# Kernel tuning notes

Hardware: AMD Instinct MI355X
Metric: run time of the kernel (lower is better)

Reference implementation:

```python
import jax, jax.numpy as jnp
import numpy as np

EMB_DIM = 1024
H = 16
HEAD_DIM = EMB_DIM // H
B = 2
S = 2048  # enc and dec seq len
LN_EPS = 1e-5


def setup_inputs() -> dict:
    key = jax.random.key(0)
    ks = jax.random.split(key, 8)
    scale_in = 1.0 / np.sqrt(EMB_DIM)
    scale_o = 1.0 / np.sqrt(H * HEAD_DIM)
    return {
        "enc_out": jax.random.normal(ks[0], (B, S, EMB_DIM), jnp.float32),
        "dec_out": jax.random.normal(ks[1], (B, S, EMB_DIM), jnp.float32),
        # stacked per-head projections, equivalent to h separate Linear(emb_dim, head_dim, bias=False)
        "Wq": jax.random.uniform(ks[2], (H, EMB_DIM, HEAD_DIM), jnp.float32, -scale_in, scale_in),
        "Wk": jax.random.uniform(ks[3], (H, EMB_DIM, HEAD_DIM), jnp.float32, -scale_in, scale_in),
        "Wv": jax.random.uniform(ks[4], (H, EMB_DIM, HEAD_DIM), jnp.float32, -scale_in, scale_in),
        "Wo": jax.random.uniform(ks[5], (H * HEAD_DIM, EMB_DIM), jnp.float32, -scale_o, scale_o),
        "gamma": jnp.ones((EMB_DIM,), jnp.float32),
        "beta": jnp.zeros((EMB_DIM,), jnp.float32),
    }


def reference(enc_out, dec_out, Wq, Wk, Wv, Wo, gamma, beta):
    d = Wq.shape[-1]
    # per-head projections, batched over heads (same math as the Python loop)
    q = jnp.einsum('bse,hed->bhsd', dec_out, Wq)   # queries from decoder
    k = jnp.einsum('bte,hed->bhtd', enc_out, Wk)   # keys from encoder
    v = jnp.einsum('bte,hed->bhtd', enc_out, Wv)   # values from encoder
    scores = jnp.einsum('bhsd,bhtd->bhst', q, k) / jnp.sqrt(jnp.asarray(d, q.dtype))
    att = jax.nn.softmax(scores, axis=-1)
    ctx = jnp.einsum('bhst,bhtd->bhsd', att, v)
    b, h, s, hd = ctx.shape
    ctx = ctx.transpose(0, 2, 1, 3).reshape(b, s, h * hd)  # concat heads along feature dim
    transformed = ctx @ Wo  # dropout is identity in eval mode
    x = dec_out + transformed
    mu = jnp.mean(x, axis=-1, keepdims=True)
    var = jnp.mean(jnp.square(x - mu), axis=-1, keepdims=True)
    return (x - mu) * jax.lax.rsqrt(var + LN_EPS) * gamma + beta
```

## Files before the change

### kernel.cpp

```cpp
#include <hip/hip_runtime.h>
#include <hip/hip_bf16.h>

#define EMB   1024
#define NH    16
#define HD    64
#define SEQ   2048
#define SA    72

typedef __attribute__((ext_vector_type(8))) short          bf16x8;
typedef __attribute__((ext_vector_type(8))) unsigned short us8;
typedef __attribute__((ext_vector_type(4))) float          f32x4;

__device__ __forceinline__ float u2f(unsigned short u) {
    return __uint_as_float(((unsigned)u) << 16);
}
__device__ __forceinline__ unsigned short f2u(float f) {
    __hip_bfloat16 b = __float2bfloat16(f);
    return *reinterpret_cast<unsigned short*>(&b);
}
__device__ __forceinline__ bool detect_bf16(const void* gamma) {
    return ((const unsigned short*)gamma)[0] == 0x3F80;
}
__device__ __forceinline__ f32x4 fzero() {
    f32x4 v; v.x = v.y = v.z = v.w = 0.f; return v;
}
__device__ __forceinline__ void ld16f(const void* p, size_t idx, bool isbf, float* o) {
    if (isbf) {
        const unsigned short* b = (const unsigned short*)p + idx;
        us8 v0 = *(const us8*)b, v1 = *(const us8*)(b + 8);
        #pragma unroll
        for (int i = 0; i < 8; ++i) { o[i] = u2f(v0[i]); o[8 + i] = u2f(v1[i]); }
    } else {
        const float* f = (const float*)p + idx;
        #pragma unroll
        for (int i = 0; i < 4; ++i) {
            float4 v = *(const float4*)(f + 4 * i);
            o[4*i] = v.x; o[4*i+1] = v.y; o[4*i+2] = v.z; o[4*i+3] = v.w;
        }
    }
}
__device__ __forceinline__ float ld1f(const void* p, size_t i, bool isbf) {
    return isbf ? u2f(((const unsigned short*)p)[i]) : ((const float*)p)[i];
}
__device__ __forceinline__ float4 ld4(const void* p, size_t idx, bool isbf) {
    if (isbf) {
        ushort4 t = *reinterpret_cast<const ushort4*>((const unsigned short*)p + idx);
        return make_float4(u2f(t.x), u2f(t.y), u2f(t.z), u2f(t.w));
    }
    return *reinterpret_cast<const float4*>((const float*)p + idx);
}
__device__ __forceinline__ us8 pk8(const float* s) {
    us8 v;
    #pragma unroll
    for (int i = 0; i < 8; ++i) v[i] = f2u(s[i]);
    return v;
}
__device__ __forceinline__ f32x4 mfma16(bf16x8 a, bf16x8 b, f32x4 c) {
    return __builtin_amdgcn_mfma_f32_16x16x32_bf16(a, b, c, 0, 0, 0);
}
__device__ __forceinline__ bf16x8 mk8(unsigned w0, unsigned w1, unsigned w2, unsigned w3) {
    union { unsigned u[4]; bf16x8 v; } x;
    x.u[0] = w0; x.u[1] = w1; x.u[2] = w2; x.u[3] = w3;
    return x.v;
}
__device__ __forceinline__ float fexp2(float x) {
    return __builtin_amdgcn_exp2f(x);
}
__device__ __forceinline__ unsigned cvtpk(float lo, float hi) {
    unsigned r;
    asm("v_cvt_pk_bf16_f32 %0, %1, %2" : "=v"(r) : "v"(lo), "v"(hi));
    return r;
}
__device__ __forceinline__ void gl_lds16(const unsigned short* g, unsigned short* l) {
    __builtin_amdgcn_global_load_lds(
        (const __attribute__((address_space(1))) void*)g,
        (__attribute__((address_space(3))) void*)l,
        16, 0, 0);
}

#define QSCALE 0.18033688f

__global__ __launch_bounds__(256) void convert_x_kernel(
    const void* __restrict__ dec, const void* __restrict__ enc,
    const void* __restrict__ gamma, unsigned short* __restrict__ xb)
{
    const bool isbf = detect_bf16(gamma);
    const size_t HALF = (size_t)4096 * 1024;
    size_t idx = ((size_t)blockIdx.x * 256 + threadIdx.x) * 16;
    const void* src; size_t off;
    if (idx < HALF) { src = dec; off = idx; } else { src = enc; off = idx - HALF; }
    float buf[16];
    ld16f(src, off, isbf, buf);
    *(us8*)&xb[idx]     = pk8(buf);
    *(us8*)&xb[idx + 8] = pk8(buf + 8);
}

__global__ __launch_bounds__(256) void transpose_w_kernel(
    const void* __restrict__ Wq, const void* __restrict__ Wk,
    const void* __restrict__ Wv, const void* __restrict__ gamma,
    unsigned short* __restrict__ wt)
{
    const bool isbf = detect_bf16(gamma);
    const int which = blockIdx.z, h = blockIdx.y, e0 = blockIdx.x * 64;
    const void* W = (which == 0) ? Wq : (which == 1 ? Wk : Wv);

    __shared__ unsigned short T[64][SA];
    const int sr = threadIdx.x >> 2, sc = (threadIdx.x & 3) * 16;

    float buf[16];
    ld16f(W, ((size_t)h * EMB + e0 + sr) * HD + sc, isbf, buf);
    #pragma unroll
    for (int i = 0; i < 16; ++i) T[sc + i][sr] = f2u(buf[i]);
    __syncthreads();
    us8 v0 = *(const us8*)&T[sr][sc];
    us8 v1 = *(const us8*)&T[sr][sc + 8];
    size_t o = (((size_t)which * NH + h) * HD + sr) * EMB + e0 + sc;
    *(us8*)&wt[o] = v0;
    *(us8*)&wt[o + 8] = v1;
}

__global__ __launch_bounds__(256) void transpose_wo_kernel(
    const void* __restrict__ Wo, const void* __restrict__ gamma,
    unsigned short* __restrict__ wot)
{
    const bool isbf = detect_bf16(gamma);
    const int n0 = blockIdx.x * 64, k0 = blockIdx.y * 64;
    __shared__ unsigned short T[64][SA];
    const int sr = threadIdx.x >> 2, sc = (threadIdx.x & 3) * 16;

    float buf[16];
    ld16f(Wo, (size_t)(k0 + sr) * EMB + n0 + sc, isbf, buf);
    #pragma unroll
    for (int i = 0; i < 16; ++i) T[sc + i][sr] = f2u(buf[i]);
    __syncthreads();
    us8 v0 = *(const us8*)&T[sr][sc];
    us8 v1 = *(const us8*)&T[sr][sc + 8];
    size_t o = (size_t)(n0 + sr) * EMB + k0 + sc;
    *(us8*)&wot[o] = v0;
    *(us8*)&wot[o + 8] = v1;
}

__global__ __launch_bounds__(256) void qkv_kernel(
    const unsigned short* __restrict__ xb,
    const unsigned short* __restrict__ wt,
    unsigned short* __restrict__ qo, unsigned short* __restrict__ ko,
    unsigned short* __restrict__ vt)
{
    const int id = blockIdx.x;
    const int xcd = id & 7, sl = id >> 3;
    const int m_t = xcd * 4 + (sl & 3);
    const int n_t = sl >> 2;
    const int m0 = m_t * 128, n0g = n_t * 128;
    const int which = n0g >> 10;
    const int nloc = n0g & 1023;
    const unsigned short* X = xb + ((which == 0) ? (size_t)0 : (size_t)4096 * 1024);

    __shared__ unsigned short smem[17408];
    unsigned short* const ldsA = smem;
    unsigned short* const ldsB = smem + 8192;

    const int tid = threadIdx.x, wv = tid >> 6, lane = tid & 63;
    const int lq = lane >> 4, lm = lane & 15;
    const int mw = (wv & 1) * 64, nw = (wv >> 1) * 64;

    const unsigned short* Wb = wt + (size_t)(which * 1024 + nloc) * EMB;

    const int seg0 = wv * 4;
    const int srow = lane >> 3;
    const int su   = (lane & 7) ^ srow;
    const unsigned short* aP[4];
    const unsigned short* bP[4];
    #pragma unroll
    for (int q = 0; q < 4; ++q) {
        const int s = seg0 + q;
        aP[q] = X  + (size_t)(m0 + 8 * s + srow) * EMB + su * 8;
        bP[q] = Wb + (size_t)(8 * s + srow) * EMB + su * 8;
    }

    f32x4 acc[4][4];
    #pragma unroll
    for (int i = 0; i < 4; ++i)
        #pragma unroll
        for (int j = 0; j < 4; ++j) acc[i][j] = fzero();

    const int xa = lm & 7;

    for (int k0 = 0; k0 < EMB; k0 += 64) {
        #pragma unroll
        for (int q = 0; q < 4; ++q) {
            gl_lds16(aP[q] + k0, ldsA + (seg0 + q) * 512);
            gl_lds16(bP[q] + k0, ldsB + (seg0 + q) * 512);
        }
        asm volatile("s_waitcnt vmcnt(0)" ::: "memory");
        __syncthreads();

        #pragma unroll
        for (int st = 0; st < 2; ++st) {
            const int u = (st * 4 + lq) ^ xa;
            bf16x8 af[4], bq[4];
            #pragma unroll
            for (int i = 0; i < 4; ++i)
                af[i] = *(const bf16x8*)(ldsA + (mw + i * 16 + lm) * 64 + u * 8);
            #pragma unroll
            for (int j = 0; j < 4; ++j)
                bq[j] = *(const bf16x8*)(ldsB + (nw + j * 16 + lm) * 64 + u * 8);
            #pragma unroll
            for (int i = 0; i < 4; ++i)
                #pragma unroll
                for (int j = 0; j < 4; ++j)
                    acc[i][j] = mfma16(af[i], bq[j], acc[i][j]);
        }
        __syncthreads();
    }

    const int b = m0 >> 11, s0 = m0 & (SEQ - 1);
    const float osc = (which == 0) ? QSCALE : 1.0f;
    if (which != 2) {
        unsigned short* Y = which ? ko : qo;
        #pragma unroll
        for (int i = 0; i < 4; ++i)
            #pragma unroll
            for (int j = 0; j < 4; ++j)
                #pragma unroll
                for (int r = 0; r < 4; ++r) {
                    int m = mw + i * 16 + lq * 4 + r;
                    int n = nloc + nw + j * 16 + lm;
                    int h = n >> 6, d = n & 63;
                    Y[(((size_t)b * NH + h) * SEQ + s0 + m) * HD + d] = f2u(acc[i][j][r] * osc);
                }
    } else {
        __syncthreads();
        unsigned short* vbuf = smem;
        #pragma unroll
        for (int i = 0; i < 4; ++i)
            #pragma unroll
            for (int j = 0; j < 4; ++j) {
                ushort4 p;
                p.x = f2u(acc[i][j][0]); p.y = f2u(acc[i][j][1]);
                p.z = f2u(acc[i][j][2]); p.w = f2u(acc[i][j][3]);
                *(ushort4*)&vbuf[(size_t)(nw + j * 16 + lm) * 136 + mw + i * 16 + lq * 4] = p;
            }
        __syncthreads();
        const int dd = tid >> 1, cc = (tid & 1) * 64;
        const int n = nloc + dd, h = n >> 6, d = n & 63;
        size_t o = (((size_t)b * NH + h) * HD + d) * SEQ + s0 + cc;
        #pragma unroll
        for (int jj = 0; jj < 8; ++jj)
            *(us8*)&vt[o + 8 * jj] = *(const us8*)&vbuf[(size_t)dd * 136 + cc + 8 * jj];
    }
}

__global__ __launch_bounds__(128) void attn_kernel(
    const unsigned short* __restrict__ qg,
    const unsigned short* __restrict__ kg,
    const unsigned short* __restrict__ vtg,
    unsigned short* __restrict__ ctx)
{
    __shared__ unsigned short Ks[2][4096];
    __shared__ unsigned short Vt[2][4096];

    const int tid = threadIdx.x, wv = tid >> 6, lane = tid & 63;
    const int lq = lane >> 4, lm = lane & 15;
    const int bh = blockIdx.x, q0 = blockIdx.y * 64;
    const unsigned short* Kg = kg + (size_t)bh * SEQ * HD;
    const unsigned short* Vg = vtg + (size_t)bh * HD * SEQ;

    const int srow = lane >> 3;
    const int su   = (lane & 7) ^ srow;
    const unsigned short* kSp[4];
    const unsigned short* vSp[4];
    #pragma unroll
    for (int j = 0; j < 4; ++j) {
        const int seg = wv + 2 * j;
        kSp[j] = Kg + (size_t)(8 * seg + srow) * HD  + su * 8;
        vSp[j] = Vg + (size_t)(8 * seg + srow) * SEQ + su * 8;
    }

    bf16x8 qf[2][2];
    #pragma unroll
    for (int s = 0; s < 2; ++s)
        #pragma unroll
        for (int st = 0; st < 2; ++st)
            qf[s][st] = *(const bf16x8*)(qg + (size_t)bh * SEQ * HD
                          + (size_t)(q0 + wv * 32 + s * 16 + lm) * HD + st * 32 + lq * 8);

    bf16x8 onesf;
    #pragma unroll
    for (int i = 0; i < 8; ++i) onesf[i] = (short)0x3F80;

    f32x4 Of[2][4], lacc[2];
    #pragma unroll
    for (int s = 0; s < 2; ++s) {
        lacc[s] = fzero();
        #pragma unroll
        for (int t = 0; t < 4; ++t) Of[s][t] = fzero();
    }

    const int xa = lm & 7;

    #pragma unroll
    for (int j = 0; j < 4; ++j) {
        gl_lds16(kSp[j], &Ks[0][(wv + 2 * j) * 512]);
        gl_lds16(vSp[j], &Vt[0][(wv + 2 * j) * 512]);
    }

    for (int it = 0; it < SEQ / 64; ++it) {
        const int cur = it & 1;
        if (it + 1 < SEQ / 64) {
            const size_t ko = (size_t)(it + 1) * 64 * HD;
            const int    vo = (it + 1) * 64;
            #pragma unroll
            for (int j = 0; j < 4; ++j) {
                gl_lds16(kSp[j] + ko, &Ks[cur ^ 1][(wv + 2 * j) * 512]);
                gl_lds16(vSp[j] + vo, &Vt[cur ^ 1][(wv + 2 * j) * 512]);
            }
            asm volatile("s_waitcnt vmcnt(8)" ::: "memory");
        } else {
            asm volatile("s_waitcnt vmcnt(0)" ::: "memory");
        }
        __syncthreads();

        f32x4 sf[2][4];
        #pragma unroll
        for (int s = 0; s < 2; ++s)
            #pragma unroll
            for (int t = 0; t < 4; ++t) sf[s][t] = fzero();
        __builtin_amdgcn_s_setprio(1);
        #pragma unroll
        for (int st = 0; st < 2; ++st) {
            const int u = (st * 4 + lq) ^ xa;
            #pragma unroll
            for (int tt = 0; tt < 4; ++tt) {
                bf16x8 kf = *(const bf16x8*)&Ks[cur][(lm + 16 * tt) * 64 + u * 8];
                sf[0][tt] = mfma16(kf, qf[0][st], sf[0][tt]);
                sf[1][tt] = mfma16(kf, qf[1][st], sf[1][tt]);
            }
        }
        __builtin_amdgcn_s_setprio(0);

        unsigned pw[2][4][2];
        #pragma unroll
        for (int s = 0; s < 2; ++s)
            #pragma unroll
            for (int tt = 0; tt < 4; ++tt) {
                pw[s][tt][0] = cvtpk(fexp2(sf[s][tt][0]), fexp2(sf[s][tt][1]));
                pw[s][tt][1] = cvtpk(fexp2(sf[s][tt][2]), fexp2(sf[s][tt][3]));
            }
        #pragma unroll
        for (int s = 0; s < 2; ++s)
            #pragma unroll
            for (int a = 0; a < 2; ++a)
                #pragma unroll
                for (int c = 0; c < 2; ++c)
                    asm("v_permlane32_swap_b32 %0, %1"
                        : "+v"(pw[s][2 * a][c]), "+v"(pw[s][2 * a + 1][c]));
        #pragma unroll
        for (int s = 0; s < 2; ++s)
            #pragma unroll
            for (int a = 0; a < 2; ++a)
                #pragma unroll
                for (int c = 0; c < 2; ++c)
                    asm("v_permlane16_swap_b32 %0, %1"
                        : "+v"(pw[s][2 * a][c]), "+v"(pw[s][2 * a + 1][c]));

        __builtin_amdgcn_s_setprio(1);
        #pragma unroll
        for (int st = 0; st < 2; ++st) {
            const int u = (st * 4 + lq) ^ xa;
            bf16x8 pf0 = mk8(pw[0][2 * st][0], pw[0][2 * st][1],
                             pw[0][2 * st + 1][0], pw[0][2 * st + 1][1]);
            bf16x8 pf1 = mk8(pw[1][2 * st][0], pw[1][2 * st][1],
                             pw[1][2 * st + 1][0], pw[1][2 * st + 1][1]);
            #pragma unroll
            for (int t = 0; t < 4; ++t) {
                bf16x8 vf = *(const bf16x8*)&Vt[cur][(lm + 16 * t) * 64 + u * 8];
                Of[0][t] = mfma16(pf0, vf, Of[0][t]);
                Of[1][t] = mfma16(pf1, vf, Of[1][t]);
            }
            lacc[0] = mfma16(pf0, onesf, lacc[0]);
            lacc[1] = mfma16(pf1, onesf, lacc[1]);
        }
        __builtin_amdgcn_s_setprio(0);
        __syncthreads();
    }

    const int b = bh >> 4, h = bh & 15;
    #pragma unroll
    for (int s = 0; s < 2; ++s)
        #pragma unroll
        for (int r = 0; r < 4; ++r) {
            float inv = 1.0f / lacc[s][r];
            int srow2 = q0 + wv * 32 + s * 16 + lq * 4 + r;
            #pragma unroll
            for (int t = 0; t < 4; ++t) {
                int d = lm + 16 * t;
                ctx[((size_t)b * SEQ + srow2) * EMB + h * HD + d] = f2u(Of[s][t][r] * inv);
            }
        }
}

__global__ __launch_bounds__(256) void oproj_kernel(
    const unsigned short* __restrict__ ctx,
    const unsigned short* __restrict__ wot,
    const void* __restrict__ dec, const void* __restrict__ gamma,
    float* __restrict__ x)
{
    const bool isbf = detect_bf16(gamma);
    const int id = blockIdx.x;
    const int xcd = id & 7, sl = id >> 3;
    const int m0 = (xcd * 4 + (sl & 3)) * 128;
    const int n0 = (sl >> 2) * 128;

    __shared__ unsigned short smem[16384];
    unsigned short* const ldsA = smem;
    unsigned short* const ldsB = smem + 8192;

    const int tid = threadIdx.x, wv = tid >> 6, lane = tid & 63;
    const int lq = lane >> 4, lm = lane & 15;
    const int mw = (wv & 1) * 64, nw = (wv >> 1) * 64;

    const int seg0 = wv * 4;
    const int srow = lane >> 3;
    const int su   = (lane & 7) ^ srow;
    const unsigned short* aP[4];
    const unsigned short* bP[4];
    #pragma unroll
    for (int q = 0; q < 4; ++q) {
        const int s = seg0 + q;
        aP[q] = ctx + (size_t)(m0 + 8 * s + srow) * EMB + su * 8;
        bP[q] = wot + (size_t)(n0 + 8 * s + srow) * EMB + su * 8;
    }

    f32x4 acc[4][4];
    #pragma unroll
    for (int i = 0; i < 4; ++i)
        #pragma unroll
        for (int j = 0; j < 4; ++j) acc[i][j] = fzero();

    const int xa = lm & 7;

    for (int k0 = 0; k0 < EMB; k0 += 64) {
        #pragma unroll
        for (int q = 0; q < 4; ++q) {
            gl_lds16(aP[q] + k0, ldsA + (seg0 + q) * 512);
            gl_lds16(bP[q] + k0, ldsB + (seg0 + q) * 512);
        }
        asm volatile("s_waitcnt vmcnt(0)" ::: "memory");
        __syncthreads();

        #pragma unroll
        for (int st = 0; st < 2; ++st) {
            const int u = (st * 4 + lq) ^ xa;
            bf16x8 af[4], bq[4];
            #pragma unroll
            for (int i = 0; i < 4; ++i)
                af[i] = *(const bf16x8*)(ldsA + (mw + i * 16 + lm) * 64 + u * 8);
            #pragma unroll
            for (int j = 0; j < 4; ++j)
                bq[j] = *(const bf16x8*)(ldsB + (nw + j * 16 + lm) * 64 + u * 8);
            #pragma unroll
            for (int i = 0; i < 4; ++i)
                #pragma unroll
                for (int j = 0; j < 4; ++j)
                    acc[i][j] = mfma16(af[i], bq[j], acc[i][j]);
        }
        __syncthreads();
    }

    #pragma unroll
    for (int i = 0; i < 4; ++i)
        #pragma unroll
        for (int j = 0; j < 4; ++j)
            #pragma unroll
            for (int r = 0; r < 4; ++r) {
                int m = m0 + mw + i * 16 + lq * 4 + r;
                int n = n0 + nw + j * 16 + lm;
                x[(size_t)m * EMB + n] = acc[i][j][r] + ld1f(dec, (size_t)m * EMB + n, isbf);
            }
}

__global__ __launch_bounds__(256) void ln_kernel(
    const float* __restrict__ x,
    const void* __restrict__ gamma,
    const void* __restrict__ beta,
    void* __restrict__ out)
{
    const bool isbf = detect_bf16(gamma);
    const int row = blockIdx.x;
    const int tid = threadIdx.x;
    const float* xr = x + (size_t)row * EMB;

    float4 xv = *reinterpret_cast<const float4*>(&xr[tid * 4]);
    float s1 = xv.x + xv.y + xv.z + xv.w;
    float s2 = xv.x * xv.x + xv.y * xv.y + xv.z * xv.z + xv.w * xv.w;

    #pragma unroll
    for (int off = 32; off > 0; off >>= 1) {
        s1 += __shfl_down(s1, off);
        s2 += __shfl_down(s2, off);
    }
    __shared__ float w1[4], w2[4];
    const int wid = tid >> 6, lane = tid & 63;
    if (lane == 0) { w1[wid] = s1; w2[wid] = s2; }
    __syncthreads();
    s1 = w1[0] + w1[1] + w1[2] + w1[3];
    s2 = w2[0] + w2[1] + w2[2] + w2[3];

    const float mu  = s1 * (1.0f / EMB);
    const float var = s2 * (1.0f / EMB) - mu * mu;
    const float rs  = rsqrtf(var + 1e-5f);

    float4 gv = ld4(gamma, (size_t)tid * 4, isbf);
    float4 bv = ld4(beta,  (size_t)tid * 4, isbf);
    float4 r;
    r.x = (xv.x - mu) * rs * gv.x + bv.x;
    r.y = (xv.y - mu) * rs * gv.y + bv.y;
    r.z = (xv.z - mu) * rs * gv.z + bv.z;
    r.w = (xv.w - mu) * rs * gv.w + bv.w;

    size_t o = (size_t)row * EMB + tid * 4;
    if (isbf) {
        ushort4 w;
        w.x = f2u(r.x); w.y = f2u(r.y); w.z = f2u(r.z); w.w = f2u(r.w);
        *reinterpret_cast<ushort4*>((unsigned short*)out + o) = w;
    } else {
        *reinterpret_cast<float4*>((float*)out + o) = r;
    }
}

extern "C" void kernel_launch(void* const* d_in, const int* in_sizes, int n_in,
                              void* d_out, int out_size, void* d_ws, size_t ws_size,
                              hipStream_t stream)
{
    const void* enc   = d_in[0];
    const void* dec   = d_in[1];
    const void* Wq    = d_in[2];
    const void* Wk    = d_in[3];
    const void* Wv    = d_in[4];
    const void* Wo    = d_in[5];
    const void* gamma = d_in[6];
    const void* beta  = d_in[7];

    char* w = (char*)d_ws;
    unsigned short* qws  = (unsigned short*)(w);
    unsigned short* kws  = (unsigned short*)(w + (size_t)8  * 1024 * 1024);
    unsigned short* vtws = (unsigned short*)(w + (size_t)16 * 1024 * 1024);
    unsigned short* wotw = (unsigned short*)(w + (size_t)16 * 1024 * 1024);
    unsigned short* wtws = (unsigned short*)(w + (size_t)24 * 1024 * 1024);
    unsigned short* cws  = (unsigned short*)(w + (size_t)24 * 1024 * 1024);
    float*          xws  = (float*)         (w);
    unsigned short* xbuf = (unsigned short*)d_out;

    convert_x_kernel   <<<2048,            256, 0, stream>>>(dec, enc, gamma, xbuf);
    transpose_w_kernel <<<dim3(16, 16, 3), 256, 0, stream>>>(Wq, Wk, Wv, gamma, wtws);
    qkv_kernel         <<<768,             256, 0, stream>>>(xbuf, wtws, qws, kws, vtws);
    attn_kernel        <<<dim3(32, 32),    128, 0, stream>>>(qws, kws, vtws, cws);
    transpose_wo_kernel<<<dim3(16, 16),    256, 0, stream>>>(Wo, gamma, wotw);
    oproj_kernel       <<<256,             256, 0, stream>>>(cws, wotw, dec, gamma, xws);
    ln_kernel          <<<4096,            256, 0, stream>>>(xws, gamma, beta, d_out);
}
```

Measured before the change: 241.7 us.

## Merge prep kernels into one launch and restructure attention loop sync

Combines the input conversion and the two weight-transpose kernels into a single prep kernel dispatched by block index, cutting two launches. Moves the Wo transpose buffer to its own workspace slot and places the context buffer in the output buffer. Reworks the attention inner loop: one full vmcnt(0) wait and barrier now sit at the top of each iteration instead of a partial wait plus a trailing barrier, the first QK MFMA uses a zero accumulator directly, and the s_setprio hints are dropped. The stricter wait can reduce how much the next tile's loads overlap with compute.

New measurement: 249.9 us. 3.4% more time.

```diff
diff --git a/kernel.cpp b/kernel.cpp
--- a/kernel.cpp
+++ b/kernel.cpp
@@ -80,64 +80,60 @@
 
 #define QSCALE 0.18033688f
 
-__global__ __launch_bounds__(256) void convert_x_kernel(
+__global__ __launch_bounds__(256) void prep_kernel(
     const void* __restrict__ dec, const void* __restrict__ enc,
-    const void* __restrict__ gamma, unsigned short* __restrict__ xb)
-{
-    const bool isbf = detect_bf16(gamma);
-    const size_t HALF = (size_t)4096 * 1024;
-    size_t idx = ((size_t)blockIdx.x * 256 + threadIdx.x) * 16;
-    const void* src; size_t off;
-    if (idx < HALF) { src = dec; off = idx; } else { src = enc; off = idx - HALF; }
-    float buf[16];
-    ld16f(src, off, isbf, buf);
-    *(us8*)&xb[idx]     = pk8(buf);
-    *(us8*)&xb[idx + 8] = pk8(buf + 8);
-}
-
-__global__ __launch_bounds__(256) void transpose_w_kernel(
     const void* __restrict__ Wq, const void* __restrict__ Wk,
-    const void* __restrict__ Wv, const void* __restrict__ gamma,
-    unsigned short* __restrict__ wt)
-{
-    const bool isbf = detect_bf16(gamma);
-    const int which = blockIdx.z, h = blockIdx.y, e0 = blockIdx.x * 64;
-    const void* W = (which == 0) ? Wq : (which == 1 ? Wk : Wv);
-
-    __shared__ unsigned short T[64][SA];
-    const int sr = threadIdx.x >> 2, sc = (threadIdx.x & 3) * 16;
-
-    float buf[16];
-    ld16f(W, ((size_t)h * EMB + e0 + sr) * HD + sc, isbf, buf);
-    #pragma unroll
-    for (int i = 0; i < 16; ++i) T[sc + i][sr] = f2u(buf[i]);
-    __syncthreads();
-    us8 v0 = *(const us8*)&T[sr][sc];
-    us8 v1 = *(const us8*)&T[sr][sc + 8];
-    size_t o = (((size_t)which * NH + h) * HD + sr) * EMB + e0 + sc;
-    *(us8*)&wt[o] = v0;
-    *(us8*)&wt[o + 8] = v1;
-}
-
-__global__ __launch_bounds__(256) void transpose_wo_kernel(
-    const void* __restrict__ Wo, const void* __restrict__ gamma,
+    const void* __restrict__ Wv, const void* __restrict__ Wo,
+    const void* __restrict__ gamma,
+    unsigned short* __restrict__ xb,
+    unsigned short* __restrict__ wt,
     unsigned short* __restrict__ wot)
 {
     const bool isbf = detect_bf16(gamma);
-    const int n0 = blockIdx.x * 64, k0 = blockIdx.y * 64;
+    const int blk = blockIdx.x;
     __shared__ unsigned short T[64][SA];
-    const int sr = threadIdx.x >> 2, sc = (threadIdx.x & 3) * 16;
-
-    float buf[16];
-    ld16f(Wo, (size_t)(k0 + sr) * EMB + n0 + sc, isbf, buf);
-    #pragma unroll
-    for (int i = 0; i < 16; ++i) T[sc + i][sr] = f2u(buf[i]);
-    __syncthreads();
-    us8 v0 = *(const us8*)&T[sr][sc];
-    us8 v1 = *(const us8*)&T[sr][sc + 8];
-    size_t o = (size_t)(n0 + sr) * EMB + k0 + sc;
-    *(us8*)&wot[o] = v0;
-    *(us8*)&wot[o + 8] = v1;
+
+    if (blk < 2048) {
+        const size_t HALF = (size_t)4096 * 1024;
+        size_t idx = ((size_t)blk * 256 + threadIdx.x) * 16;
+        const void* src; size_t off;
+        if (idx < HALF) { src = dec; off = idx; } else { src = enc; off = idx - HALF; }
+        float buf[16];
+        ld16f(src, off, isbf, buf);
+        *(us8*)&xb[idx]     = pk8(buf);
+        *(us8*)&xb[idx + 8] = pk8(buf + 8);
+    } else if (blk < 2816) {
+        const int local = blk - 2048;
+        const int which = local >> 8, h = (local >> 4) & 15, e0 = (local & 15) * 64;
+        const void* W = (which == 0) ? Wq : (which == 1 ? Wk : Wv);
+        const int sr = threadIdx.x >> 2, sc = (threadIdx.x & 3) * 16;
+
+        float buf[16];
+        ld16f(W, ((size_t)h * EMB + e0 + sr) * HD + sc, isbf, buf);
+        #pragma unroll
+        for (int i = 0; i < 16; ++i) T[sc + i][sr] = f2u(buf[i]);
+        __syncthreads();
+        us8 v0 = *(const us8*)&T[sr][sc];
+        us8 v1 = *(const us8*)&T[sr][sc + 8];
+        size_t o = (((size_t)which * NH + h) * HD + sr) * EMB + e0 + sc;
+        *(us8*)&wt[o] = v0;
+        *(us8*)&wt[o + 8] = v1;
+    } else {
+        const int local = blk - 2816;
+        const int n0 = (local & 15) * 64, k0 = (local >> 4) * 64;
+        const int sr = threadIdx.x >> 2, sc = (threadIdx.x & 3) * 16;
+
+        float buf[16];
+        ld16f(Wo, (size_t)(k0 + sr) * EMB + n0 + sc, isbf, buf);
+        #pragma unroll
+        for (int i = 0; i < 16; ++i) T[sc + i][sr] = f2u(buf[i]);
+        __syncthreads();
+        us8 v0 = *(const us8*)&T[sr][sc];
+        us8 v1 = *(const us8*)&T[sr][sc + 8];
+        size_t o = (size_t)(n0 + sr) * EMB + k0 + sc;
+        *(us8*)&wot[o] = v0;
+        *(us8*)&wot[o + 8] = v1;
+    }
 }
 
 __global__ __launch_bounds__(256) void qkv_kernel(
@@ -288,6 +284,7 @@
     #pragma unroll
     for (int i = 0; i < 8; ++i) onesf[i] = (short)0x3F80;
 
+    const f32x4 z = fzero();
     f32x4 Of[2][4], lacc[2];
     #pragma unroll
     for (int s = 0; s < 2; ++s) {
@@ -297,6 +294,8 @@
     }
 
     const int xa = lm & 7;
+    const int u0 = lq ^ xa;
+    const int u1 = (4 + lq) ^ xa;
 
     #pragma unroll
     for (int j = 0; j < 4; ++j) {
@@ -306,6 +305,8 @@
 
     for (int it = 0; it < SEQ / 64; ++it) {
         const int cur = it & 1;
+        asm volatile("s_waitcnt vmcnt(0)" ::: "memory");
+        __syncthreads();
         if (it + 1 < SEQ / 64) {
             const size_t ko = (size_t)(it + 1) * 64 * HD;
             const int    vo = (it + 1) * 64;
@@ -314,29 +315,21 @@
                 gl_lds16(kSp[j] + ko, &Ks[cur ^ 1][(wv + 2 * j) * 512]);
                 gl_lds16(vSp[j] + vo, &Vt[cur ^ 1][(wv + 2 * j) * 512]);
             }
-            asm volatile("s_waitcnt vmcnt(8)" ::: "memory");
-        } else {
-            asm volatile("s_waitcnt vmcnt(0)" ::: "memory");
-        }
-        __syncthreads();
+        }
 
         f32x4 sf[2][4];
         #pragma unroll
-        for (int s = 0; s < 2; ++s)
-            #pragma unroll
-            for (int t = 0; t < 4; ++t) sf[s][t] = fzero();
-        __builtin_amdgcn_s_setprio(1);
-        #pragma unroll
-        for (int st = 0; st < 2; ++st) {
-            const int u = (st * 4 + lq) ^ xa;
-            #pragma unroll
-            for (int tt = 0; tt < 4; ++tt) {
-                bf16x8 kf = *(const bf16x8*)&Ks[cur][(lm + 16 * tt) * 64 + u * 8];
-                sf[0][tt] = mfma16(kf, qf[0][st], sf[0][tt]);
-                sf[1][tt] = mfma16(kf, qf[1][st], sf[1][tt]);
-            }
-        }
-        __builtin_amdgcn_s_setprio(0);
+        for (int tt = 0; tt < 4; ++tt) {
+            bf16x8 kf = *(const bf16x8*)&Ks[cur][(lm + 16 * tt) * 64 + u0 * 8];
+            sf[0][tt] = mfma16(kf, qf[0][0], z);
+            sf[1][tt] = mfma16(kf, qf[1][0], z);
+        }
+        #pragma unroll
+        for (int tt = 0; tt < 4; ++tt) {
+            bf16x8 kf = *(const bf16x8*)&Ks[cur][(lm + 16 * tt) * 64 + u1 * 8];
+            sf[0][tt] = mfma16(kf, qf[0][1], sf[0][tt]);
+            sf[1][tt] = mfma16(kf, qf[1][1], sf[1][tt]);
+        }
 
         unsigned pw[2][4][2];
         #pragma unroll
@@ -363,10 +356,9 @@
                     asm("v_permlane16_swap_b32 %0, %1"
                         : "+v"(pw[s][2 * a][c]), "+v"(pw[s][2 * a + 1][c]));
 
-        __builtin_amdgcn_s_setprio(1);
         #pragma unroll
         for (int st = 0; st < 2; ++st) {
-            const int u = (st * 4 + lq) ^ xa;
+            const int u = st ? u1 : u0;
             bf16x8 pf0 = mk8(pw[0][2 * st][0], pw[0][2 * st][1],
                              pw[0][2 * st + 1][0], pw[0][2 * st + 1][1]);
             bf16x8 pf1 = mk8(pw[1][2 * st][0], pw[1][2 * st][1],
@@ -380,8 +372,6 @@
             lacc[0] = mfma16(pf0, onesf, lacc[0]);
             lacc[1] = mfma16(pf1, onesf, lacc[1]);
         }
-        __builtin_amdgcn_s_setprio(0);
-        __syncthreads();
     }
 
     const int b = bh >> 4, h = bh & 15;
@@ -545,17 +535,16 @@
     unsigned short* qws  = (unsigned short*)(w);
     unsigned short* kws  = (unsigned short*)(w + (size_t)8  * 1024 * 1024);
     unsigned short* vtws = (unsigned short*)(w + (size_t)16 * 1024 * 1024);
-    unsigned short* wotw = (unsigned short*)(w + (size_t)16 * 1024 * 1024);
     unsigned short* wtws = (unsigned short*)(w + (size_t)24 * 1024 * 1024);
-    unsigned short* cws  = (unsigned short*)(w + (size_t)24 * 1024 * 1024);
+    unsigned short* wotw = (unsigned short*)(w + (size_t)30 * 1024 * 1024);
     float*          xws  = (float*)         (w);
     unsigned short* xbuf = (unsigned short*)d_out;
-
-    convert_x_kernel   <<<2048,            256, 0, stream>>>(dec, enc, gamma, xbuf);
-    transpose_w_kernel <<<dim3(16, 16, 3), 256, 0, stream>>>(Wq, Wk, Wv, gamma, wtws);
-    qkv_kernel         <<<768,             256, 0, stream>>>(xbuf, wtws, qws, kws, vtws);
-    attn_kernel        <<<dim3(32, 32),    128, 0, stream>>>(qws, kws, vtws, cws);
-    transpose_wo_kernel<<<dim3(16, 16),    256, 0, stream>>>(Wo, gamma, wotw);
-    oproj_kernel       <<<256,             256, 0, stream>>>(cws, wotw, dec, gamma, xws);
-    ln_kernel          <<<4096,            256, 0, stream>>>(xws, gamma, beta, d_out);
-}
+    unsigned short* cws  = (unsigned short*)d_out;
+
+    prep_kernel  <<<3072,          256, 0, stream>>>(dec, enc, Wq, Wk, Wv, Wo,
+                                                     gamma, xbuf, wtws, wotw);
+    qkv_kernel   <<<768,           256, 0, stream>>>(xbuf, wtws, qws, kws, vtws);
+    attn_kernel  <<<dim3(32, 32),  128, 0, stream>>>(qws, kws, vtws, cws);
+    oproj_kernel <<<256,           256, 0, stream>>>(cws, wotw, dec, gamma, xws);
+    ln_kernel    <<<4096,          256, 0, stream>>>(xws, gamma, beta, d_out);
+}
```
